# Performance work log

Hardware: AMD Instinct MI355X
Metric: run time of the kernel (lower is better)

Reference implementation:

```python
import jax, jax.numpy as jnp
import numpy as np

EPS = 1e-6

def rmsnorm(x, w):
    # x * rsqrt(mean(x^2, -1) + eps) * w
    ms = jnp.mean(jnp.square(x), axis=-1, keepdims=True)
    return w * (x * jax.lax.rsqrt(ms + EPS))

def setup_inputs() -> dict:
    key = jax.random.key(0)
    ks = jax.random.split(key, 10)
    B, L, T, D, R = 4, 8, 2048, 1024, 64
    h_base = jax.random.normal(ks[0], (B, T, D), dtype=jnp.float32)
    prev_states = jax.random.normal(ks[1], (B, L, T, D), dtype=jnp.float32)
    query = jax.random.normal(ks[2], (D,), dtype=jnp.float32) * 0.02
    gate = jnp.float32(0.5)
    score_w = jnp.ones((D,), dtype=jnp.float32)
    out_w = jnp.ones((D,), dtype=jnp.float32)
    qnorm_w = jnp.ones((D,), dtype=jnp.float32)
    # low-rank query projections (nn.Linear weight layout: [out, in])
    Wd = jax.random.normal(ks[3], (R, D), dtype=jnp.float32) * 0.02
    Wu = jax.random.normal(ks[4], (D, R), dtype=jnp.float32) * 0.02
    # token gate projection
    tg_w = jax.random.normal(ks[5], (1, D), dtype=jnp.float32) * 0.02
    tg_b = jnp.zeros((1,), dtype=jnp.float32)
    return {"h_base": h_base, "prev_states": prev_states, "query": query,
            "gate": gate, "score_w": score_w, "out_w": out_w,
            "qnorm_w": qnorm_w, "Wd": Wd, "Wu": Wu, "tg_w": tg_w, "tg_b": tg_b}

def reference(h_base, prev_states, query, gate, score_w, out_w, qnorm_w, Wd, Wu, tg_w, tg_b):
    sources = prev_states                              # [B,L,T,D]
    normed = rmsnorm(sources, score_w)                 # [B,L,T,D]
    # low-rank input-dependent query: q = query + up(down(qnorm(h)))
    qh = rmsnorm(h_base, qnorm_w)                      # [B,T,D]
    q = query + jnp.einsum('btr,dr->btd', jnp.einsum('btd,rd->btr', qh, Wd), Wu)
    scores = jnp.einsum('btd,bltd->blt', q, normed)    # [B,L,T]
    alpha = jax.nn.softmax(scores, axis=1)             # softmax over depth L
    delta = jnp.einsum('blt,bltd->btd', alpha, sources)
    delta = rmsnorm(delta, out_w)                      # [B,T,D]
    g = gate * jax.nn.sigmoid(h_base @ tg_w.T + tg_b)  # [B,T,1]
    out = h_base + g * delta
    return out, alpha
```

## Files before the change

kernel.cpp:

```cpp
#include <hip/hip_runtime.h>
#include <hip/hip_bf16.h>

#define D_DIM 1024
#define L_DIM 8
#define T_DIM 2048
#define B_DIM 4
#define TOKS  (B_DIM * T_DIM)
#define OUT_ELEMS ((size_t)TOKS * D_DIM)
#define EPSF 1e-6f

typedef __attribute__((ext_vector_type(8)))  short short8_t;
typedef __attribute__((ext_vector_type(16))) float f32x16_t;
typedef __attribute__((ext_vector_type(4)))  float f32x4_t;

#define QT_STRIDE 1048

__device__ __forceinline__ float wave_sum(float v) {
#pragma unroll
    for (int off = 32; off; off >>= 1) v += __shfl_xor(v, off, 64);
    return v;
}

__device__ __forceinline__ float dot4v(const f32x4_t& a, const f32x4_t& b) {
    return a.x * b.x + a.y * b.y + a.z * b.z + a.w * b.w;
}

__device__ __forceinline__ unsigned short f2bf(float f) {
    union { __hip_bfloat16 h; unsigned short u; } x;
    x.h = __float2bfloat16(f);
    return x.u;
}

__device__ __forceinline__ float bf2f(unsigned short u) {
    union { unsigned int i; float f; } x;
    x.i = ((unsigned int)u) << 16;
    return x.f;
}

__global__ __launch_bounds__(256) void k_prep(const float* __restrict__ Wd,
                                              const float* __restrict__ qnw,
                                              const float* __restrict__ Wu,
                                              unsigned short* __restrict__ Wdq,
                                              unsigned short* __restrict__ Wubf) {
    int i = (blockIdx.x * 256 + threadIdx.x) * 4;
    float4 wd = *(const float4*)(Wd + i);
    float4 nv = *(const float4*)(qnw + (i & (D_DIM - 1)));
    short4 o1 = make_short4((short)f2bf(wd.x * nv.x), (short)f2bf(wd.y * nv.y),
                            (short)f2bf(wd.z * nv.z), (short)f2bf(wd.w * nv.w));
    *(short4*)(Wdq + i) = o1;
    float4 wu = *(const float4*)(Wu + i);
    short4 o2 = make_short4((short)f2bf(wu.x), (short)f2bf(wu.y),
                            (short)f2bf(wu.z), (short)f2bf(wu.w));
    *(short4*)(Wubf + i) = o2;
}

__global__ __launch_bounds__(512) void k_q(const float* __restrict__ h,
                                           const unsigned short* __restrict__ Wdq,
                                           const unsigned short* __restrict__ Wubf,
                                           const float* __restrict__ query,
                                           const float* __restrict__ score_w,
                                           unsigned short* __restrict__ qs) {
    __shared__ __align__(16) char smem[70784];
    float (*c_red)[2][16][64] = (float (*)[2][16][64])smem;
    float (*ssq_red)[32]      = (float (*)[32])(smem + 65536);
    float* scale_sh           = (float*)(smem + 66560);
    unsigned short* r_sw      = (unsigned short*)(smem + 66688);
    unsigned short* qt        = (unsigned short*)smem;

    int tid  = threadIdx.x;
    int w    = tid >> 6;
    int lane = tid & 63;
    int t0   = blockIdx.x * 32;

    f32x16_t acc0, acc1;
#pragma unroll
    for (int r = 0; r < 16; ++r) { acc0[r] = 0.f; acc1[r] = 0.f; }

    int arow = lane & 31;
    int koff = w * 128 + (lane >> 5) * 8;
    const float* hrow = h + (size_t)(t0 + arow) * D_DIM + koff;
    const unsigned short* b0 = Wdq + (size_t)arow * D_DIM + koff;
    const unsigned short* b1 = Wdq + (size_t)(32 + arow) * D_DIM + koff;

    float ssq = 0.f;
#pragma unroll
    for (int s = 0; s < 8; ++s) {
        f32x4_t ha = *(const f32x4_t*)(hrow + s * 16);
        f32x4_t hb = *(const f32x4_t*)(hrow + s * 16 + 4);
        ssq += dot4v(ha, ha) + dot4v(hb, hb);
        short8_t af;
        af[0] = (short)f2bf(ha.x); af[1] = (short)f2bf(ha.y);
        af[2] = (short)f2bf(ha.z); af[3] = (short)f2bf(ha.w);
        af[4] = (short)f2bf(hb.x); af[5] = (short)f2bf(hb.y);
        af[6] = (short)f2bf(hb.z); af[7] = (short)f2bf(hb.w);
        short8_t bf0 = *(const short8_t*)(b0 + s * 16);
        short8_t bf1 = *(const short8_t*)(b1 + s * 16);
        acc0 = __builtin_amdgcn_mfma_f32_32x32x16_bf16(af, bf0, acc0, 0, 0, 0);
        acc1 = __builtin_amdgcn_mfma_f32_32x32x16_bf16(af, bf1, acc1, 0, 0, 0);
    }

    ssq += __shfl_xor(ssq, 32, 64);
    if (lane < 32) ssq_red[w][lane] = ssq;
#pragma unroll
    for (int r = 0; r < 16; ++r) {
        c_red[w][0][r][lane] = acc0[r];
        c_red[w][1][r][lane] = acc1[r];
    }
    __syncthreads();

    if (tid < 32) {
        float s8 = 0.f;
#pragma unroll
        for (int u = 0; u < 8; ++u) s8 += ssq_red[u][tid];
        scale_sh[tid] = rsqrtf(s8 * (1.f / D_DIM) + EPSF);
    }
    __syncthreads();

    for (int idx = tid; idx < 2048; idx += 512) {
        int nj = idx >> 10, rem = idx & 1023, reg = rem >> 6, ln = rem & 63;
        float v = 0.f;
#pragma unroll
        for (int u = 0; u < 8; ++u) v += c_red[u][nj][reg][ln];
        int tk = (reg & 3) + 8 * (reg >> 2) + 4 * (ln >> 5);
        int j  = nj * 32 + (ln & 31);
        v *= scale_sh[tk];
        int byte = (tk * 128 + j * 2) ^ ((tk & 7) << 4);
        r_sw[byte >> 1] = f2bf(v);
    }
    __syncthreads();

    short8_t afr[4];
#pragma unroll
    for (int s = 0; s < 4; ++s) {
        int tk = lane & 31;
        int k  = s * 16 + (lane >> 5) * 8;
        int byte = (tk * 128 + k * 2) ^ ((tk & 7) << 4);
        afr[s] = *(const short8_t*)(&r_sw[byte >> 1]);
    }
    __syncthreads();

#pragma unroll
    for (int i = 0; i < 4; ++i) {
        int n0 = (w * 4 + i) * 32;
        int d  = n0 + (lane & 31);
        f32x16_t c;
#pragma unroll
        for (int r = 0; r < 16; ++r) c[r] = 0.f;
        const unsigned short* bb = Wubf + (size_t)d * 64 + (lane >> 5) * 8;
#pragma unroll
        for (int s = 0; s < 4; ++s) {
            short8_t bf = *(const short8_t*)(bb + s * 16);
            c = __builtin_amdgcn_mfma_f32_32x32x16_bf16(afr[s], bf, c, 0, 0, 0);
        }
        float qd  = query[d];
        float swd = score_w[d];
#pragma unroll
        for (int r = 0; r < 16; ++r) {
            int tk = (r & 3) + 8 * (r >> 2) + 4 * (lane >> 5);
            unsigned int v = f2bf((qd + c[r]) * swd);
            unsigned int pv = (unsigned int)__shfl_xor((int)v, 1, 64);
            if ((lane & 1) == 0) {
                unsigned int word = (v & 0xffffu) | (pv << 16);
                *(unsigned int*)&qt[tk * QT_STRIDE + d] = word;
            }
        }
    }
    __syncthreads();

#pragma unroll
    for (int j = 0; j < 8; ++j) {
        int row   = tid >> 4;
        int chunk = (tid & 15) + j * 16;
        short8_t v = *(const short8_t*)&qt[row * QT_STRIDE + chunk * 8];
        *(short8_t*)(qs + (size_t)(t0 + row) * D_DIM + chunk * 8) = v;
    }
}

__global__ __launch_bounds__(256) void k_main(const float* __restrict__ h,
                                              const float* __restrict__ prev,
                                              const unsigned short* __restrict__ qs,
                                              const float* __restrict__ out_w,
                                              const float* __restrict__ tg_w,
                                              const float* __restrict__ gate,
                                              const float* __restrict__ tg_b,
                                              float* __restrict__ out,
                                              float* __restrict__ alpha_out) {
    __shared__ float red[16][264];
    __shared__ float fin[16];
    __shared__ float gred[4];
    __shared__ float dred[4];

    int tid = threadIdx.x, lane = tid & 63, w = tid >> 6;
    int blk = blockIdx.x;
    int b   = blk >> 11;
    int t   = blk & (T_DIM - 1);
    size_t tok = (size_t)blk;

    const float* pbase = prev + ((size_t)(b * L_DIM) * T_DIM + t) * D_DIM;
    f32x4_t p[L_DIM];
#pragma unroll
    for (int l = 0; l < L_DIM; ++l)
        p[l] = __builtin_nontemporal_load(((const f32x4_t*)(pbase + (size_t)l * T_DIM * D_DIM)) + tid);

    f32x4_t h4 = ((const f32x4_t*)(h + tok * D_DIM))[tid];
    short4 qraw = *(const short4*)(qs + tok * D_DIM + tid * 4);
    f32x4_t qv;
    qv.x = bf2f((unsigned short)qraw.x);
    qv.y = bf2f((unsigned short)qraw.y);
    qv.z = bf2f((unsigned short)qraw.z);
    qv.w = bf2f((unsigned short)qraw.w);
    f32x4_t tw = ((const f32x4_t*)tg_w)[tid];

    float gp = wave_sum(dot4v(h4, tw));
    if (lane == 0) gred[w] = gp;

#pragma unroll
    for (int l = 0; l < L_DIM; ++l) {
        red[l][tid]     = dot4v(p[l], p[l]);
        red[l + 8][tid] = dot4v(p[l], qv);
    }
    __syncthreads();

    {
        int v = tid >> 4, seg = tid & 15;
        float s = 0.f;
#pragma unroll
        for (int i = 0; i < 16; ++i) s += red[v][seg + 16 * i];
#pragma unroll
        for (int off = 1; off < 16; off <<= 1) s += __shfl_xor(s, off, 64);
        if (seg == 0) fin[v] = s;
    }
    __syncthreads();

    float sc[L_DIM], mx = -1e30f;
#pragma unroll
    for (int l = 0; l < L_DIM; ++l) {
        sc[l] = fin[l + 8] * rsqrtf(fin[l] * (1.f / D_DIM) + EPSF);
        mx = fmaxf(mx, sc[l]);
    }
    float al[L_DIM], asum = 0.f;
#pragma unroll
    for (int l = 0; l < L_DIM; ++l) { al[l] = __expf(sc[l] - mx); asum += al[l]; }
    float inv = 1.f / asum;
#pragma unroll
    for (int l = 0; l < L_DIM; ++l) al[l] *= inv;

    float gd = gred[0] + gred[1] + gred[2] + gred[3];
    float g  = gate[0] / (1.f + __expf(-(gd + tg_b[0])));

    f32x4_t dl = {0.f, 0.f, 0.f, 0.f};
#pragma unroll
    for (int l = 0; l < L_DIM; ++l) {
        dl.x += al[l] * p[l].x; dl.y += al[l] * p[l].y;
        dl.z += al[l] * p[l].z; dl.w += al[l] * p[l].w;
    }
    float dss = wave_sum(dot4v(dl, dl));
    if (lane == 0) dred[w] = dss;
    __syncthreads();
    float dsum   = dred[0] + dred[1] + dred[2] + dred[3];
    float dscale = rsqrtf(dsum * (1.f / D_DIM) + EPSF);

    f32x4_t ow = ((const f32x4_t*)out_w)[tid];
    f32x4_t o;
    o.x = h4.x + g * dl.x * dscale * ow.x;
    o.y = h4.y + g * dl.y * dscale * ow.y;
    o.z = h4.z + g * dl.z * dscale * ow.z;
    o.w = h4.w + g * dl.w * dscale * ow.w;
    __builtin_nontemporal_store(o, ((f32x4_t*)(out + tok * D_DIM)) + tid);

    if (tid < L_DIM)
        alpha_out[(size_t)b * (L_DIM * T_DIM) + tid * T_DIM + t] = al[tid];
}

extern "C" void kernel_launch(void* const* d_in, const int* in_sizes, int n_in,
                              void* d_out, int out_size, void* d_ws, size_t ws_size,
                              hipStream_t stream) {
    (void)in_sizes; (void)n_in; (void)out_size; (void)ws_size;
    const float* h       = (const float*)d_in[0];
    const float* prev    = (const float*)d_in[1];
    const float* query   = (const float*)d_in[2];
    const float* gate    = (const float*)d_in[3];
    const float* score_w = (const float*)d_in[4];
    const float* out_w   = (const float*)d_in[5];
    const float* qnw     = (const float*)d_in[6];
    const float* Wd      = (const float*)d_in[7];
    const float* Wu      = (const float*)d_in[8];
    const float* tg_w    = (const float*)d_in[9];
    const float* tg_b    = (const float*)d_in[10];

    float* out   = (float*)d_out;
    float* alpha = out + OUT_ELEMS;

    unsigned short* qsbuf = (unsigned short*)d_ws;
    unsigned short* Wdq   = qsbuf + OUT_ELEMS;
    unsigned short* Wubf  = Wdq + (size_t)64 * D_DIM;

    k_prep<<<64, 256, 0, stream>>>(Wd, qnw, Wu, Wdq, Wubf);
    k_q<<<TOKS / 32, 512, 0, stream>>>(h, Wdq, Wubf, query, score_w, qsbuf);
    k_main<<<TOKS, 256, 0, stream>>>(h, prev, qsbuf, out_w, tg_w, gate, tg_b, out, alpha);
}
```

Before: 90.44 us.

## Fuse query projection and depth attention into one per-32-token kernel

Merges the low-rank query kernel and the main depth-softmax kernel into one kernel, so the bf16 query stays in shared memory and the workspace round trip is removed. The token-gate dot product moves into the first phase, computed alongside the RMS sum of squares. Each block then walks its 32 tokens in sequence, prefetching the previous-state rows for the next token (double buffering) and doing three block-wide reductions per token. The grid shrinks to 256 large blocks, which trades global parallelism and memory-level parallelism for the streaming prev_states read against the saved intermediate traffic and launch.

```diff
diff --git a/kernel.cpp b/kernel.cpp
--- a/kernel.cpp
+++ b/kernel.cpp
@@ -12,14 +12,7 @@
 typedef __attribute__((ext_vector_type(8)))  short short8_t;
 typedef __attribute__((ext_vector_type(16))) float f32x16_t;
 typedef __attribute__((ext_vector_type(4)))  float f32x4_t;
-
-#define QT_STRIDE 1048
-
-__device__ __forceinline__ float wave_sum(float v) {
-#pragma unroll
-    for (int off = 32; off; off >>= 1) v += __shfl_xor(v, off, 64);
-    return v;
-}
+typedef __attribute__((ext_vector_type(2)))  float f32x2_t;
 
 __device__ __forceinline__ float dot4v(const f32x4_t& a, const f32x4_t& b) {
     return a.x * b.x + a.y * b.y + a.z * b.z + a.w * b.w;
@@ -54,18 +47,31 @@
     *(short4*)(Wubf + i) = o2;
 }
 
-__global__ __launch_bounds__(512) void k_q(const float* __restrict__ h,
-                                           const unsigned short* __restrict__ Wdq,
-                                           const unsigned short* __restrict__ Wubf,
-                                           const float* __restrict__ query,
-                                           const float* __restrict__ score_w,
-                                           unsigned short* __restrict__ qs) {
-    __shared__ __align__(16) char smem[70784];
+__global__ __launch_bounds__(512) void k_fused(const float* __restrict__ h,
+                                               const float* __restrict__ prev,
+                                               const unsigned short* __restrict__ Wdq,
+                                               const unsigned short* __restrict__ Wubf,
+                                               const float* __restrict__ query,
+                                               const float* __restrict__ score_w,
+                                               const float* __restrict__ out_w,
+                                               const float* __restrict__ tg_w,
+                                               const float* __restrict__ gate,
+                                               const float* __restrict__ tg_b,
+                                               float* __restrict__ out,
+                                               float* __restrict__ alpha_out) {
+    __shared__ __align__(16) char smem[65536];
     float (*c_red)[2][16][64] = (float (*)[2][16][64])smem;
-    float (*ssq_red)[32]      = (float (*)[32])(smem + 65536);
-    float* scale_sh           = (float*)(smem + 66560);
-    unsigned short* r_sw      = (unsigned short*)(smem + 66688);
-    unsigned short* qt        = (unsigned short*)smem;
+    unsigned short* qt = (unsigned short*)smem;
+
+    __shared__ float ssq_red[8][32];
+    __shared__ float tg_red[8][32];
+    __shared__ float scale_sh[32];
+    __shared__ float g_sh[32];
+    __shared__ float alpha_sh[8][33];
+    __shared__ unsigned short r_sw[2048];
+    __shared__ float red[16][136];
+    __shared__ float red2[136];
+    __shared__ float fin[16];
 
     int tid  = threadIdx.x;
     int w    = tid >> 6;
@@ -81,13 +87,17 @@
     const float* hrow = h + (size_t)(t0 + arow) * D_DIM + koff;
     const unsigned short* b0 = Wdq + (size_t)arow * D_DIM + koff;
     const unsigned short* b1 = Wdq + (size_t)(32 + arow) * D_DIM + koff;
-
-    float ssq = 0.f;
+    const float* tgb = tg_w + koff;
+
+    float ssq = 0.f, tgp = 0.f;
 #pragma unroll
     for (int s = 0; s < 8; ++s) {
         f32x4_t ha = *(const f32x4_t*)(hrow + s * 16);
         f32x4_t hb = *(const f32x4_t*)(hrow + s * 16 + 4);
         ssq += dot4v(ha, ha) + dot4v(hb, hb);
+        f32x4_t ta = *(const f32x4_t*)(tgb + s * 16);
+        f32x4_t tb = *(const f32x4_t*)(tgb + s * 16 + 4);
+        tgp += dot4v(ha, ta) + dot4v(hb, tb);
         short8_t af;
         af[0] = (short)f2bf(ha.x); af[1] = (short)f2bf(ha.y);
         af[2] = (short)f2bf(ha.z); af[3] = (short)f2bf(ha.w);
@@ -100,7 +110,8 @@
     }
 
     ssq += __shfl_xor(ssq, 32, 64);
-    if (lane < 32) ssq_red[w][lane] = ssq;
+    tgp += __shfl_xor(tgp, 32, 64);
+    if (lane < 32) { ssq_red[w][lane] = ssq; tg_red[w][lane] = tgp; }
 #pragma unroll
     for (int r = 0; r < 16; ++r) {
         c_red[w][0][r][lane] = acc0[r];
@@ -109,10 +120,11 @@
     __syncthreads();
 
     if (tid < 32) {
-        float s8 = 0.f;
-#pragma unroll
-        for (int u = 0; u < 8; ++u) s8 += ssq_red[u][tid];
+        float s8 = 0.f, t8 = 0.f;
+#pragma unroll
+        for (int u = 0; u < 8; ++u) { s8 += ssq_red[u][tid]; t8 += tg_red[u][tid]; }
         scale_sh[tid] = rsqrtf(s8 * (1.f / D_DIM) + EPSF);
+        g_sh[tid] = gate[0] / (1.f + __expf(-(t8 + tg_b[0])));
     }
     __syncthreads();
 
@@ -146,10 +158,10 @@
         f32x16_t c;
 #pragma unroll
         for (int r = 0; r < 16; ++r) c[r] = 0.f;
-        const unsigned short* bb = Wubf + (size_t)d * 64 + (lane >> 5) * 8;
+        const unsigned short* bbp = Wubf + (size_t)d * 64 + (lane >> 5) * 8;
 #pragma unroll
         for (int s = 0; s < 4; ++s) {
-            short8_t bf = *(const short8_t*)(bb + s * 16);
+            short8_t bf = *(const short8_t*)(bbp + s * 16);
             c = __builtin_amdgcn_mfma_f32_32x32x16_bf16(afr[s], bf, c, 0, 0, 0);
         }
         float qd  = query[d];
@@ -161,115 +173,114 @@
             unsigned int pv = (unsigned int)__shfl_xor((int)v, 1, 64);
             if ((lane & 1) == 0) {
                 unsigned int word = (v & 0xffffu) | (pv << 16);
-                *(unsigned int*)&qt[tk * QT_STRIDE + d] = word;
+                *(unsigned int*)&qt[tk * 1024 + d] = word;
             }
         }
     }
     __syncthreads();
 
-#pragma unroll
-    for (int j = 0; j < 8; ++j) {
-        int row   = tid >> 4;
-        int chunk = (tid & 15) + j * 16;
-        short8_t v = *(const short8_t*)&qt[row * QT_STRIDE + chunk * 8];
-        *(short8_t*)(qs + (size_t)(t0 + row) * D_DIM + chunk * 8) = v;
-    }
-}
-
-__global__ __launch_bounds__(256) void k_main(const float* __restrict__ h,
-                                              const float* __restrict__ prev,
-                                              const unsigned short* __restrict__ qs,
-                                              const float* __restrict__ out_w,
-                                              const float* __restrict__ tg_w,
-                                              const float* __restrict__ gate,
-                                              const float* __restrict__ tg_b,
-                                              float* __restrict__ out,
-                                              float* __restrict__ alpha_out) {
-    __shared__ float red[16][264];
-    __shared__ float fin[16];
-    __shared__ float gred[4];
-    __shared__ float dred[4];
-
-    int tid = threadIdx.x, lane = tid & 63, w = tid >> 6;
-    int blk = blockIdx.x;
-    int b   = blk >> 11;
-    int t   = blk & (T_DIM - 1);
-    size_t tok = (size_t)blk;
-
-    const float* pbase = prev + ((size_t)(b * L_DIM) * T_DIM + t) * D_DIM;
-    f32x4_t p[L_DIM];
-#pragma unroll
-    for (int l = 0; l < L_DIM; ++l)
-        p[l] = __builtin_nontemporal_load(((const f32x4_t*)(pbase + (size_t)l * T_DIM * D_DIM)) + tid);
-
-    f32x4_t h4 = ((const f32x4_t*)(h + tok * D_DIM))[tid];
-    short4 qraw = *(const short4*)(qs + tok * D_DIM + tid * 4);
-    f32x4_t qv;
-    qv.x = bf2f((unsigned short)qraw.x);
-    qv.y = bf2f((unsigned short)qraw.y);
-    qv.z = bf2f((unsigned short)qraw.z);
-    qv.w = bf2f((unsigned short)qraw.w);
-    f32x4_t tw = ((const f32x4_t*)tg_w)[tid];
-
-    float gp = wave_sum(dot4v(h4, tw));
-    if (lane == 0) gred[w] = gp;
-
-#pragma unroll
-    for (int l = 0; l < L_DIM; ++l) {
-        red[l][tid]     = dot4v(p[l], p[l]);
-        red[l + 8][tid] = dot4v(p[l], qv);
-    }
-    __syncthreads();
-
-    {
-        int v = tid >> 4, seg = tid & 15;
-        float s = 0.f;
-#pragma unroll
-        for (int i = 0; i < 16; ++i) s += red[v][seg + 16 * i];
-#pragma unroll
-        for (int off = 1; off < 16; off <<= 1) s += __shfl_xor(s, off, 64);
-        if (seg == 0) fin[v] = s;
-    }
-    __syncthreads();
-
-    float sc[L_DIM], mx = -1e30f;
-#pragma unroll
-    for (int l = 0; l < L_DIM; ++l) {
-        sc[l] = fin[l + 8] * rsqrtf(fin[l] * (1.f / D_DIM) + EPSF);
-        mx = fmaxf(mx, sc[l]);
-    }
-    float al[L_DIM], asum = 0.f;
-#pragma unroll
-    for (int l = 0; l < L_DIM; ++l) { al[l] = __expf(sc[l] - mx); asum += al[l]; }
-    float inv = 1.f / asum;
-#pragma unroll
-    for (int l = 0; l < L_DIM; ++l) al[l] *= inv;
-
-    float gd = gred[0] + gred[1] + gred[2] + gred[3];
-    float g  = gate[0] / (1.f + __expf(-(gd + tg_b[0])));
-
-    f32x4_t dl = {0.f, 0.f, 0.f, 0.f};
-#pragma unroll
-    for (int l = 0; l < L_DIM; ++l) {
-        dl.x += al[l] * p[l].x; dl.y += al[l] * p[l].y;
-        dl.z += al[l] * p[l].z; dl.w += al[l] * p[l].w;
-    }
-    float dss = wave_sum(dot4v(dl, dl));
-    if (lane == 0) dred[w] = dss;
-    __syncthreads();
-    float dsum   = dred[0] + dred[1] + dred[2] + dred[3];
-    float dscale = rsqrtf(dsum * (1.f / D_DIM) + EPSF);
-
-    f32x4_t ow = ((const f32x4_t*)out_w)[tid];
-    f32x4_t o;
-    o.x = h4.x + g * dl.x * dscale * ow.x;
-    o.y = h4.y + g * dl.y * dscale * ow.y;
-    o.z = h4.z + g * dl.z * dscale * ow.z;
-    o.w = h4.w + g * dl.w * dscale * ow.w;
-    __builtin_nontemporal_store(o, ((f32x4_t*)(out + tok * D_DIM)) + tid);
-
-    if (tid < L_DIM)
-        alpha_out[(size_t)b * (L_DIM * T_DIM) + tid * T_DIM + t] = al[tid];
+    int tloc0 = t0 & (T_DIM - 1);
+    int bb    = t0 >> 11;
+    int d0    = tid * 2;
+    const float* pb0 = prev + ((size_t)bb * L_DIM * T_DIM + tloc0) * D_DIM + d0;
+    const float* hb0 = h + (size_t)t0 * D_DIM + d0;
+    float*       ob0 = out + (size_t)t0 * D_DIM + d0;
+    f32x2_t ow2 = *(const f32x2_t*)(out_w + d0);
+
+    f32x2_t pA[8], pB[8];
+    f32x2_t hA, hB;
+    unsigned int qA, qB;
+
+    auto LOADP = [&](int t, f32x2_t (&p)[8], f32x2_t& h2, unsigned int& qr) {
+#pragma unroll
+        for (int l = 0; l < 8; ++l)
+            p[l] = __builtin_nontemporal_load(
+                (const f32x2_t*)(pb0 + ((size_t)l * T_DIM + t) * D_DIM));
+        h2 = *(const f32x2_t*)(hb0 + (size_t)t * D_DIM);
+        qr = *(const unsigned int*)&qt[t * 1024 + d0];
+    };
+
+    auto PROCESS = [&](int t, f32x2_t (&p)[8], f32x2_t h2, unsigned int qr) {
+        float qlo = bf2f((unsigned short)(qr & 0xffffu));
+        float qhi = bf2f((unsigned short)(qr >> 16));
+        float ss[8], dt[8];
+#pragma unroll
+        for (int l = 0; l < 8; ++l) {
+            ss[l] = p[l].x * p[l].x + p[l].y * p[l].y;
+            dt[l] = p[l].x * qlo + p[l].y * qhi;
+        }
+#pragma unroll
+        for (int l = 0; l < 8; ++l) {
+            ss[l] += __shfl_xor(ss[l], 1, 64); ss[l] += __shfl_xor(ss[l], 2, 64);
+            dt[l] += __shfl_xor(dt[l], 1, 64); dt[l] += __shfl_xor(dt[l], 2, 64);
+        }
+        if ((tid & 3) == 0) {
+            int e = tid >> 2;
+#pragma unroll
+            for (int l = 0; l < 8; ++l) { red[l][e] = ss[l]; red[l + 8][e] = dt[l]; }
+        }
+        __syncthreads();
+        {
+            int v = tid >> 5, e = tid & 31;
+            float s = red[v][e] + red[v][e + 32] + red[v][e + 64] + red[v][e + 96];
+            s += __shfl_xor(s, 1, 64);  s += __shfl_xor(s, 2, 64);
+            s += __shfl_xor(s, 4, 64);  s += __shfl_xor(s, 8, 64);
+            s += __shfl_xor(s, 16, 64);
+            if (e == 0) fin[v] = s;
+        }
+        __syncthreads();
+        float al[8];
+        float mx = -1e30f;
+#pragma unroll
+        for (int l = 0; l < 8; ++l) {
+            al[l] = fin[l + 8] * rsqrtf(fin[l] * (1.f / D_DIM) + EPSF);
+            mx = fmaxf(mx, al[l]);
+        }
+        float asum = 0.f;
+#pragma unroll
+        for (int l = 0; l < 8; ++l) { al[l] = __expf(al[l] - mx); asum += al[l]; }
+        float inv = 1.f / asum;
+        float dx = 0.f, dy = 0.f;
+#pragma unroll
+        for (int l = 0; l < 8; ++l) { al[l] *= inv; dx += al[l] * p[l].x; dy += al[l] * p[l].y; }
+#pragma unroll
+        for (int l = 0; l < 8; ++l) if (tid == l) alpha_sh[l][t] = al[l];
+        float dsp = dx * dx + dy * dy;
+        dsp += __shfl_xor(dsp, 1, 64); dsp += __shfl_xor(dsp, 2, 64);
+        if ((tid & 3) == 0) red2[tid >> 2] = dsp;
+        __syncthreads();
+        {
+            int e = tid & 31;
+            float s = red2[e] + red2[e + 32] + red2[e + 64] + red2[e + 96];
+            s += __shfl_xor(s, 1, 64);  s += __shfl_xor(s, 2, 64);
+            s += __shfl_xor(s, 4, 64);  s += __shfl_xor(s, 8, 64);
+            s += __shfl_xor(s, 16, 64);
+            float dscale = rsqrtf(s * (1.f / D_DIM) + EPSF);
+            float g = g_sh[t];
+            f32x2_t o;
+            o.x = h2.x + g * dx * dscale * ow2.x;
+            o.y = h2.y + g * dy * dscale * ow2.y;
+            __builtin_nontemporal_store(o, (f32x2_t*)(ob0 + (size_t)t * D_DIM));
+        }
+    };
+
+    LOADP(0, pA, hA, qA);
+#pragma unroll 1
+    for (int t = 0; t < 32; t += 2) {
+        if (t + 1 < 32) LOADP(t + 1, pB, hB, qB);
+        PROCESS(t, pA, hA, qA);
+        if (t + 2 < 32) LOADP(t + 2, pA, hA, qA);
+        PROCESS(t + 1, pB, hB, qB);
+    }
+
+    __syncthreads();
+    if (tid < 64) {
+        int l = tid >> 3, c = (tid & 7) * 4;
+        float4 v;
+        v.x = alpha_sh[l][c];     v.y = alpha_sh[l][c + 1];
+        v.z = alpha_sh[l][c + 2]; v.w = alpha_sh[l][c + 3];
+        *(float4*)(alpha_out + (size_t)bb * (L_DIM * T_DIM) + (size_t)l * T_DIM + tloc0 + c) = v;
+    }
 }
 
 extern "C" void kernel_launch(void* const* d_in, const int* in_sizes, int n_in,
@@ -291,11 +302,10 @@
     float* out   = (float*)d_out;
     float* alpha = out + OUT_ELEMS;
 
-    unsigned short* qsbuf = (unsigned short*)d_ws;
-    unsigned short* Wdq   = qsbuf + OUT_ELEMS;
-    unsigned short* Wubf  = Wdq + (size_t)64 * D_DIM;
+    unsigned short* Wdq  = (unsigned short*)d_ws;
+    unsigned short* Wubf = Wdq + (size_t)64 * D_DIM;
 
     k_prep<<<64, 256, 0, stream>>>(Wd, qnw, Wu, Wdq, Wubf);
-    k_q<<<TOKS / 32, 512, 0, stream>>>(h, Wdq, Wubf, query, score_w, qsbuf);
-    k_main<<<TOKS, 256, 0, stream>>>(h, prev, qsbuf, out_w, tg_w, gate, tg_b, out, alpha);
-}
+    k_fused<<<256, 512, 0, stream>>>(h, prev, Wdq, Wubf, query, score_w, out_w,
+                                     tg_w, gate, tg_b, out, alpha);
+}
```

Measured after the change: 118.3 us. 1.31x slower.

## Process one token per wavefront in k_main to eliminate LDS reductions and barriers

Applied to the files above, without the earlier changes.

k_main now assigns one token per 64-lane wavefront (four tokens per block) instead of one token per 256-thread block. Each lane holds 16 floats per depth level, and all reductions (sum of squares, score dot products, gate dot, delta norm) become wave-level shuffles, with no shared memory and no __syncthreads. The cost is far higher register pressure, about 128 floats for the prev values alone, which may lower occupancy and the number of loads in flight on this memory-bound kernel.

```diff
diff --git a/kernel.cpp b/kernel.cpp
--- a/kernel.cpp
+++ b/kernel.cpp
@@ -12,14 +12,6 @@
 typedef __attribute__((ext_vector_type(8)))  short short8_t;
 typedef __attribute__((ext_vector_type(16))) float f32x16_t;
 typedef __attribute__((ext_vector_type(4)))  float f32x4_t;
-
-#define QT_STRIDE 1048
-
-__device__ __forceinline__ float wave_sum(float v) {
-#pragma unroll
-    for (int off = 32; off; off >>= 1) v += __shfl_xor(v, off, 64);
-    return v;
-}
 
 __device__ __forceinline__ float dot4v(const f32x4_t& a, const f32x4_t& b) {
     return a.x * b.x + a.y * b.y + a.z * b.z + a.w * b.w;
@@ -54,6 +46,7 @@
     *(short4*)(Wubf + i) = o2;
 }
 
+#define QT_STRIDE 1048
 __global__ __launch_bounds__(512) void k_q(const float* __restrict__ h,
                                            const unsigned short* __restrict__ Wdq,
                                            const unsigned short* __restrict__ Wubf,
@@ -146,10 +139,10 @@
         f32x16_t c;
 #pragma unroll
         for (int r = 0; r < 16; ++r) c[r] = 0.f;
-        const unsigned short* bb = Wubf + (size_t)d * 64 + (lane >> 5) * 8;
+        const unsigned short* bbp = Wubf + (size_t)d * 64 + (lane >> 5) * 8;
 #pragma unroll
         for (int s = 0; s < 4; ++s) {
-            short8_t bf = *(const short8_t*)(bb + s * 16);
+            short8_t bf = *(const short8_t*)(bbp + s * 16);
             c = __builtin_amdgcn_mfma_f32_32x32x16_bf16(afr[s], bf, c, 0, 0, 0);
         }
         float qd  = query[d];
@@ -185,91 +178,111 @@
                                               const float* __restrict__ tg_b,
                                               float* __restrict__ out,
                                               float* __restrict__ alpha_out) {
-    __shared__ float red[16][264];
-    __shared__ float fin[16];
-    __shared__ float gred[4];
-    __shared__ float dred[4];
-
-    int tid = threadIdx.x, lane = tid & 63, w = tid >> 6;
-    int blk = blockIdx.x;
-    int b   = blk >> 11;
-    int t   = blk & (T_DIM - 1);
-    size_t tok = (size_t)blk;
-
-    const float* pbase = prev + ((size_t)(b * L_DIM) * T_DIM + t) * D_DIM;
-    f32x4_t p[L_DIM];
+    int lane = threadIdx.x & 63;
+    int tok  = (blockIdx.x << 2) + (threadIdx.x >> 6);
+    int b    = tok >> 11;
+    int t    = tok & (T_DIM - 1);
+
+    const float* pb = prev + ((size_t)(b * L_DIM) * T_DIM + t) * D_DIM + lane * 4;
+    f32x4_t p[L_DIM][4];
 #pragma unroll
     for (int l = 0; l < L_DIM; ++l)
-        p[l] = __builtin_nontemporal_load(((const f32x4_t*)(pbase + (size_t)l * T_DIM * D_DIM)) + tid);
-
-    f32x4_t h4 = ((const f32x4_t*)(h + tok * D_DIM))[tid];
-    short4 qraw = *(const short4*)(qs + tok * D_DIM + tid * 4);
-    f32x4_t qv;
-    qv.x = bf2f((unsigned short)qraw.x);
-    qv.y = bf2f((unsigned short)qraw.y);
-    qv.z = bf2f((unsigned short)qraw.z);
-    qv.w = bf2f((unsigned short)qraw.w);
-    f32x4_t tw = ((const f32x4_t*)tg_w)[tid];
-
-    float gp = wave_sum(dot4v(h4, tw));
-    if (lane == 0) gred[w] = gp;
-
+#pragma unroll
+        for (int c = 0; c < 4; ++c)
+            p[l][c] = __builtin_nontemporal_load(
+                (const f32x4_t*)(pb + (size_t)l * T_DIM * D_DIM + c * 256));
+
+    const float* hb = h + (size_t)tok * D_DIM + lane * 4;
+    f32x4_t h4[4], qv[4];
+#pragma unroll
+    for (int c = 0; c < 4; ++c) h4[c] = *(const f32x4_t*)(hb + c * 256);
+#pragma unroll
+    for (int c = 0; c < 4; ++c) {
+        short4 qr = *(const short4*)(qs + (size_t)tok * D_DIM + c * 256 + lane * 4);
+        qv[c].x = bf2f((unsigned short)qr.x);
+        qv[c].y = bf2f((unsigned short)qr.y);
+        qv[c].z = bf2f((unsigned short)qr.z);
+        qv[c].w = bf2f((unsigned short)qr.w);
+    }
+
+    float tgp = 0.f;
+#pragma unroll
+    for (int c = 0; c < 4; ++c) {
+        f32x4_t tw = *(const f32x4_t*)(tg_w + c * 256 + lane * 4);
+        tgp += dot4v(h4[c], tw);
+    }
+
+    float ss[L_DIM], dt[L_DIM];
 #pragma unroll
     for (int l = 0; l < L_DIM; ++l) {
-        red[l][tid]     = dot4v(p[l], p[l]);
-        red[l + 8][tid] = dot4v(p[l], qv);
-    }
-    __syncthreads();
-
-    {
-        int v = tid >> 4, seg = tid & 15;
-        float s = 0.f;
-#pragma unroll
-        for (int i = 0; i < 16; ++i) s += red[v][seg + 16 * i];
-#pragma unroll
-        for (int off = 1; off < 16; off <<= 1) s += __shfl_xor(s, off, 64);
-        if (seg == 0) fin[v] = s;
-    }
-    __syncthreads();
-
-    float sc[L_DIM], mx = -1e30f;
+        float s = 0.f, d = 0.f;
+#pragma unroll
+        for (int c = 0; c < 4; ++c) {
+            s += dot4v(p[l][c], p[l][c]);
+            d += dot4v(p[l][c], qv[c]);
+        }
+        ss[l] = s; dt[l] = d;
+    }
+
+#pragma unroll
+    for (int off = 32; off; off >>= 1) {
+#pragma unroll
+        for (int l = 0; l < L_DIM; ++l) {
+            ss[l] += __shfl_xor(ss[l], off, 64);
+            dt[l] += __shfl_xor(dt[l], off, 64);
+        }
+        tgp += __shfl_xor(tgp, off, 64);
+    }
+
+    float al[L_DIM], mx = -1e30f;
 #pragma unroll
     for (int l = 0; l < L_DIM; ++l) {
-        sc[l] = fin[l + 8] * rsqrtf(fin[l] * (1.f / D_DIM) + EPSF);
-        mx = fmaxf(mx, sc[l]);
-    }
-    float al[L_DIM], asum = 0.f;
-#pragma unroll
-    for (int l = 0; l < L_DIM; ++l) { al[l] = __expf(sc[l] - mx); asum += al[l]; }
+        al[l] = dt[l] * rsqrtf(ss[l] * (1.f / D_DIM) + EPSF);
+        mx = fmaxf(mx, al[l]);
+    }
+    float asum = 0.f;
+#pragma unroll
+    for (int l = 0; l < L_DIM; ++l) { al[l] = __expf(al[l] - mx); asum += al[l]; }
     float inv = 1.f / asum;
 #pragma unroll
     for (int l = 0; l < L_DIM; ++l) al[l] *= inv;
 
-    float gd = gred[0] + gred[1] + gred[2] + gred[3];
-    float g  = gate[0] / (1.f + __expf(-(gd + tg_b[0])));
-
-    f32x4_t dl = {0.f, 0.f, 0.f, 0.f};
-#pragma unroll
-    for (int l = 0; l < L_DIM; ++l) {
-        dl.x += al[l] * p[l].x; dl.y += al[l] * p[l].y;
-        dl.z += al[l] * p[l].z; dl.w += al[l] * p[l].w;
-    }
-    float dss = wave_sum(dot4v(dl, dl));
-    if (lane == 0) dred[w] = dss;
-    __syncthreads();
-    float dsum   = dred[0] + dred[1] + dred[2] + dred[3];
-    float dscale = rsqrtf(dsum * (1.f / D_DIM) + EPSF);
-
-    f32x4_t ow = ((const f32x4_t*)out_w)[tid];
-    f32x4_t o;
-    o.x = h4.x + g * dl.x * dscale * ow.x;
-    o.y = h4.y + g * dl.y * dscale * ow.y;
-    o.z = h4.z + g * dl.z * dscale * ow.z;
-    o.w = h4.w + g * dl.w * dscale * ow.w;
-    __builtin_nontemporal_store(o, ((f32x4_t*)(out + tok * D_DIM)) + tid);
-
-    if (tid < L_DIM)
-        alpha_out[(size_t)b * (L_DIM * T_DIM) + tid * T_DIM + t] = al[tid];
+    float g = gate[0] / (1.f + __expf(-(tgp + tg_b[0])));
+
+    f32x4_t dl[4];
+#pragma unroll
+    for (int c = 0; c < 4; ++c) { dl[c].x = 0.f; dl[c].y = 0.f; dl[c].z = 0.f; dl[c].w = 0.f; }
+#pragma unroll
+    for (int l = 0; l < L_DIM; ++l)
+#pragma unroll
+        for (int c = 0; c < 4; ++c) {
+            dl[c].x += al[l] * p[l][c].x;
+            dl[c].y += al[l] * p[l][c].y;
+            dl[c].z += al[l] * p[l][c].z;
+            dl[c].w += al[l] * p[l][c].w;
+        }
+
+    float dss = 0.f;
+#pragma unroll
+    for (int c = 0; c < 4; ++c) dss += dot4v(dl[c], dl[c]);
+#pragma unroll
+    for (int off = 32; off; off >>= 1) dss += __shfl_xor(dss, off, 64);
+    float dscale = rsqrtf(dss * (1.f / D_DIM) + EPSF);
+
+    float* ob = out + (size_t)tok * D_DIM + lane * 4;
+#pragma unroll
+    for (int c = 0; c < 4; ++c) {
+        f32x4_t ow = *(const f32x4_t*)(out_w + c * 256 + lane * 4);
+        f32x4_t o;
+        o.x = h4[c].x + g * dl[c].x * dscale * ow.x;
+        o.y = h4[c].y + g * dl[c].y * dscale * ow.y;
+        o.z = h4[c].z + g * dl[c].z * dscale * ow.z;
+        o.w = h4[c].w + g * dl[c].w * dscale * ow.w;
+        __builtin_nontemporal_store(o, (f32x4_t*)(ob + c * 256));
+    }
+
+    if (lane < L_DIM)
+        alpha_out[(size_t)b * (L_DIM * T_DIM) + (size_t)lane * T_DIM + t] = al[lane];
 }
 
 extern "C" void kernel_launch(void* const* d_in, const int* in_sizes, int n_in,
@@ -297,5 +310,5 @@
 
     k_prep<<<64, 256, 0, stream>>>(Wd, qnw, Wu, Wdq, Wubf);
     k_q<<<TOKS / 32, 512, 0, stream>>>(h, Wdq, Wubf, query, score_w, qsbuf);
-    k_main<<<TOKS, 256, 0, stream>>>(h, prev, qsbuf, out_w, tg_w, gate, tg_b, out, alpha);
-}
+    k_main<<<TOKS / 4, 256, 0, stream>>>(h, prev, qsbuf, out_w, tg_w, gate, tg_b, out, alpha);
+}
```

New measurement: 87.10 us. 1.04x faster.
